# Performance work log

Measured on AMD Instinct MI355X. Metric: run time of the kernel, lower is better.

Reference implementation:

```python
import jax, jax.numpy as jnp
import numpy as np

E = 128   # embed_dim
H = 8     # num_heads
N, T, LQ, LK = 32, 50, 64, 64


def setup_inputs() -> dict:
    rng = jax.random.key(0)
    ks = jax.random.split(rng, 9)
    xav = np.sqrt(2.0 / (E + E)).astype(np.float32)  # xavier_normal for square E x E
    return {
        "query": jax.random.normal(ks[0], (N, T, LQ, E), jnp.float32),
        "key": jax.random.normal(ks[1], (N, T, LK, E), jnp.float32),
        "value": jax.random.normal(ks[2], (N, T, LK, E), jnp.float32),
        "key_padding_mask": jax.random.bernoulli(ks[3], 0.1, (N, T, LK)),
        "Wq": jax.random.normal(ks[4], (E, E), jnp.float32) * xav,
        "bq": jnp.zeros((E,), jnp.float32),
        "Wk": jax.random.normal(ks[5], (E, E), jnp.float32) * xav,
        "bk": jnp.zeros((E,), jnp.float32),
        "Wv": jax.random.normal(ks[6], (E, E), jnp.float32) * xav,
        "bv": jnp.zeros((E,), jnp.float32),
        "Wo": jax.random.normal(ks[7], (E, E), jnp.float32) * xav,
        "bo": jnp.zeros((E,), jnp.float32),
    }


def reference(query, key, value, key_padding_mask, Wq, bq, Wk, bk, Wv, bv, Wo, bo):
    b, t, lq, _ = query.shape
    lk = key.shape[2]
    # linear projections (torch Linear: x @ W.T + b)
    q = (query @ Wq.T + bq).reshape(b, t, lq, H, -1)   # [b,T,Lq,h,d]
    k = (key @ Wk.T + bk).reshape(b, t, lk, H, -1)     # [b,T,Lk,h,d]
    v = (value @ Wv.T + bv).reshape(b, t, lk, H, -1)   # [b,T,Lk,h,d]
    scale = 1.0 / np.sqrt(q.shape[-1]).astype(np.float32)
    attn = jnp.einsum('bTlhd,bTthd->bThlt', q, k) * scale  # [b,T,h,Lq,Lk]
    mask = key_padding_mask[:, :, None, None, :]            # [b,T,1,1,Lk]
    attn = jnp.where(mask, -jnp.inf, attn)
    attn = jax.nn.softmax(attn, axis=-1)
    attn = jnp.nan_to_num(attn, nan=0.0)                    # fully-masked rows -> 0
    out = jnp.einsum('bThlt,bTthd->bTlhd', attn, v)
    out = out.reshape(b, t, lq, -1) @ Wo.T + bo             # [b,T,Lq,E]
    # match torch output layout for attn: [head, b, T, Lq, Lk]
    return out, jnp.transpose(attn, (2, 0, 1, 3, 4))
```

## Files before the change

kernel.cpp:

```cpp
#include <hip/hip_runtime.h>
#include <hip/hip_bf16.h>


#define NBT 1600
#define OUT0_ELEMS 13107200L

typedef __attribute__((ext_vector_type(8))) short bf16x8;
typedef __attribute__((ext_vector_type(4))) short bf16x4;
typedef __attribute__((ext_vector_type(4))) float f32x4;
typedef __attribute__((ext_vector_type(4))) unsigned short u16x4;

__device__ __forceinline__ unsigned short f2b(float f) {
  union { float f; unsigned u; } v; v.f = f;
  unsigned r = v.u + 0x7FFFu + ((v.u >> 16) & 1u);
  return (unsigned short)(r >> 16);
}
__device__ __forceinline__ float b2f(unsigned short s) {
  union { unsigned u; float f; } v; v.u = ((unsigned)s) << 16;
  return v.f;
}
__device__ __forceinline__ bf16x4 pack4(f32x4 v) {
  bf16x4 r;
  r[0] = (short)f2b(v[0]); r[1] = (short)f2b(v[1]);
  r[2] = (short)f2b(v[2]); r[3] = (short)f2b(v[3]);
  return r;
}

#if defined(__has_builtin)
#if __has_builtin(__builtin_amdgcn_mfma_f32_16x16x16bf16_1k)
#define HAVE_MFMA16_1K 1
#endif
#endif

__device__ __forceinline__ f32x4 mfma16(bf16x4 a, bf16x4 b, f32x4 c) {
#ifdef HAVE_MFMA16_1K
  return __builtin_amdgcn_mfma_f32_16x16x16bf16_1k(a, b, c, 0, 0, 0);
#else
  f32x4 d;
  asm volatile("v_mfma_f32_16x16x16_bf16 %0, %1, %2, %3\n\ts_nop 7\n\ts_nop 7"
               : "=v"(d)
               : "v"(a), "v"(b), "v"(c));
  return d;
#endif
}

__device__ __forceinline__ int xs_idx(int r, int c) {
  return r * 128 + (c ^ ((r & 7) << 3));
}
__device__ __forceinline__ int qk_idx(int l, int d) {
  return l * 16 + (d ^ ((l & 3) << 2));
}
__device__ __forceinline__ int ps_idx(int r, int c) {
  return r * 64 + (c ^ ((r & 7) << 3));
}

__global__ void prep_kernel(const float* __restrict__ Wq,
                            const float* __restrict__ Wk,
                            const float* __restrict__ Wv,
                            const float* __restrict__ Wo,
                            const unsigned char* __restrict__ maskp,
                            unsigned short* __restrict__ wall,
                            int* __restrict__ flag) {
  int b = blockIdx.x;
  int t = threadIdx.x;
  if (b < 256) {
    int idx = b * 256 + t;
    int m = idx >> 14, j = idx & 16383;
    const float* src = (m == 0) ? Wq : (m == 1) ? Wk : (m == 2) ? Wv : Wo;
    float s = (m == 0) ? 0.25f : 1.0f;
    wall[idx] = f2b(src[j] * s);
  } else {
    __shared__ int sb, sf;
    if (t == 0) { sb = 0; sf = 0; }
    __syncthreads();
    int bnz = 0, fcnt = 0;
    for (int i = t * 16; i < t * 16 + 16; ++i)
      if ((i & 3) && maskp[i]) bnz++;
    const unsigned int* w = (const unsigned int*)maskp;
    for (int i = t * 4; i < t * 4 + 4; ++i)
      if (w[i] == 0x3f800000u) fcnt++;
    if (bnz) atomicAdd(&sb, 1);
    if (fcnt) atomicAdd(&sf, 1);
    __syncthreads();
    if (t == 0) *flag = sf ? 2 : (sb ? 1 : 0);
  }
}

__global__ __launch_bounds__(512, 4) void fused_kernel(
    const float* __restrict__ q_in, const float* __restrict__ k_in,
    const float* __restrict__ v_in, const unsigned char* __restrict__ maskp,
    const int* __restrict__ modeFlag, const unsigned short* __restrict__ wall,
    const float* __restrict__ bq, const float* __restrict__ bk,
    const float* __restrict__ bv, const float* __restrict__ bo,
    float* __restrict__ out0, float* __restrict__ attn_out) {
  __shared__ __align__(16) unsigned short Xs[64 * 128];
  __shared__ __align__(16) unsigned short QKw[8 * 1024];
  __shared__ float maskS[64];

  const int tid = threadIdx.x;
  const int w = tid >> 6;
  const int lane = tid & 63;
  const int ln = lane & 15, g = lane >> 4;
  const long bT = blockIdx.x;

  unsigned short* Sw = QKw + w * 1024;

  if (tid < 64) {
    int mode = *modeFlag;
    long midx = bT * 64 + tid;
    bool mk;
    if (mode == 0)      mk = ((const int*)maskp)[midx] != 0;
    else if (mode == 1) mk = maskp[midx] != 0;
    else                mk = ((const float*)maskp)[midx] != 0.0f;
    maskS[tid] = mk ? -INFINITY : 0.0f;
  }

  const float* xsrc0 = q_in + bT * 8192;
  const float* xsrc1 = k_in + bT * 8192;
  const float* xsrc2 = v_in + bT * 8192;

  float4 xcur[4];
  #pragma unroll
  for (int it = 0; it < 4; ++it)
    xcur[it] = *(const float4*)(xsrc0 + it * 2048 + tid * 4);

  bf16x4 vk[4];
  bf16x4 aK[4], bQ[4];

  #pragma unroll
  for (int t3 = 0; t3 < 3; ++t3) {
    #pragma unroll
    for (int it = 0; it < 4; ++it) {
      int flat = it * 2048 + tid * 4;
      int r = flat >> 7, c = flat & 127;
      float4 xv = xcur[it];
      u16x4 pk;
      pk[0] = f2b(xv.x); pk[1] = f2b(xv.y);
      pk[2] = f2b(xv.z); pk[3] = f2b(xv.w);
      *(u16x4*)&Xs[xs_idx(r, c)] = pk;
    }
    if (t3 < 2) {
      const float* nsrc = (t3 == 0) ? xsrc1 : xsrc2;
      #pragma unroll
      for (int it = 0; it < 4; ++it)
        xcur[it] = *(const float4*)(nsrc + it * 2048 + tid * 4);
    }
    __syncthreads();

    const unsigned short* wb = wall + t3 * 16384 + (w * 16 + ln) * 128 + 8 * g;
    const float* bias = (t3 == 0) ? bq : (t3 == 1) ? bk : bv;
    float bval = bias[w * 16 + ln] * ((t3 == 0) ? 0.25f : 1.0f);

    f32x4 acc[4] = {};
    #pragma unroll
    for (int ks = 0; ks < 4; ++ks) {
      bf16x8 bwk = *(const bf16x8*)(wb + ks * 32);
      bf16x8 a[4];
      #pragma unroll
      for (int ms = 0; ms < 4; ++ms)
        a[ms] = *(const bf16x8*)&Xs[xs_idx(ms * 16 + ln, ks * 32 + 8 * g)];
      #pragma unroll
      for (int ms = 0; ms < 4; ++ms)
        acc[ms] = __builtin_amdgcn_mfma_f32_16x16x32_bf16(a[ms], bwk,
                                                          acc[ms], 0, 0, 0);
    }
    __syncthreads();

    #pragma unroll
    for (int ms = 0; ms < 4; ++ms) {
      if (t3 == 2) {
        f32x4 vb;
        #pragma unroll
        for (int r = 0; r < 4; ++r) vb[r] = acc[ms][r] + bval;
        vk[ms] = pack4(vb);
      } else {
        #pragma unroll
        for (int r = 0; r < 4; ++r) {
          int l = ms * 16 + 4 * g + r;
          Sw[qk_idx(l, ln)] = f2b(acc[ms][r] + bval);
        }
      }
    }
    if (t3 == 0) {
      #pragma unroll
      for (int i = 0; i < 4; ++i)
        bQ[i] = *(const bf16x4*)&Sw[qk_idx(i * 16 + ln, 4 * g)];
    } else if (t3 == 1) {
      #pragma unroll
      for (int i = 0; i < 4; ++i)
        aK[i] = *(const bf16x4*)&Sw[qk_idx(i * 16 + ln, 4 * g)];
    }
  }

  const long abase = ((long)w * NBT + bT) * 4096;
  #pragma unroll
  for (int lsub = 0; lsub < 4; ++lsub) {
    f32x4 s4[4];
    #pragma unroll
    for (int t = 0; t < 4; ++t) {
      f32x4 z = {};
      s4[t] = mfma16(aK[t], bQ[lsub], z);
    }
    float m = -INFINITY;
    #pragma unroll
    for (int t = 0; t < 4; ++t) {
      f32x4 mvt = *(const f32x4*)&maskS[t * 16 + 4 * g];
      #pragma unroll
      for (int r = 0; r < 4; ++r) {
        float sv = s4[t][r] + mvt[r];
        s4[t][r] = sv;
        m = fmaxf(m, sv);
      }
    }
    m = fmaxf(m, __shfl_xor(m, 16, 64));
    m = fmaxf(m, __shfl_xor(m, 32, 64));
    float sum = 0.f;
    #pragma unroll
    for (int t = 0; t < 4; ++t)
      #pragma unroll
      for (int r = 0; r < 4; ++r) {
        float p = (m == -INFINITY) ? 0.f : __expf(s4[t][r] - m);
        s4[t][r] = p;
        sum += p;
      }
    sum += __shfl_xor(sum, 16, 64);
    sum += __shfl_xor(sum, 32, 64);
    float inv = (sum > 0.f) ? 1.f / sum : 0.f;

    bf16x4 pa4[4];
    #pragma unroll
    for (int t = 0; t < 4; ++t) {
      f32x4 ps;
      #pragma unroll
      for (int r = 0; r < 4; ++r) ps[r] = s4[t][r] * inv;
      pa4[t] = pack4(ps);
    }

    #pragma unroll
    for (int t = 0; t < 4; ++t)
      *(u16x4*)&Sw[ps_idx(ln, t * 16 + 4 * g)] = *(const u16x4*)&pa4[t];
    #pragma unroll
    for (int j = 0; j < 4; ++j) {
      int row = 4 * j + g;
      u16x4 pv = *(const u16x4*)&Sw[ps_idx(row, 4 * ln)];
      float4 o = make_float4(b2f(pv[0]), b2f(pv[1]), b2f(pv[2]), b2f(pv[3]));
      *(float4*)&attn_out[abase + (long)(lsub * 16 + row) * 64 + 4 * ln] = o;
    }

    f32x4 oacc = {};
    #pragma unroll
    for (int t = 0; t < 4; ++t) oacc = mfma16(pa4[t], vk[t], oacc);
    #pragma unroll
    for (int r = 0; r < 4; ++r)
      Xs[xs_idx(lsub * 16 + 4 * g + r, w * 16 + ln)] = f2b(oacc[r]);
  }

  __syncthreads();

  {
    const unsigned short* wo = wall + 3 * 16384 + (w * 16 + ln) * 128 + 8 * g;
    float bov = bo[w * 16 + ln];

    f32x4 acc[4] = {};
    #pragma unroll
    for (int ks = 0; ks < 4; ++ks) {
      bf16x8 bwk = *(const bf16x8*)(wo + ks * 32);
      bf16x8 a[4];
      #pragma unroll
      for (int ms = 0; ms < 4; ++ms)
        a[ms] = *(const bf16x8*)&Xs[xs_idx(ms * 16 + ln, ks * 32 + 8 * g)];
      #pragma unroll
      for (int ms = 0; ms < 4; ++ms)
        acc[ms] = __builtin_amdgcn_mfma_f32_16x16x32_bf16(a[ms], bwk,
                                                          acc[ms], 0, 0, 0);
    }
    #pragma unroll
    for (int ms = 0; ms < 4; ++ms)
      #pragma unroll
      for (int r = 0; r < 4; ++r)
        out0[(bT * 64 + ms * 16 + 4 * g + r) * 128 + w * 16 + ln] =
            acc[ms][r] + bov;
  }
}

extern "C" void kernel_launch(void* const* d_in, const int* in_sizes, int n_in,
                              void* d_out, int out_size, void* d_ws,
                              size_t ws_size, hipStream_t stream) {
  (void)in_sizes; (void)n_in; (void)out_size; (void)ws_size;
  const float* query = (const float*)d_in[0];
  const float* key   = (const float*)d_in[1];
  const float* value = (const float*)d_in[2];
  const unsigned char* mask = (const unsigned char*)d_in[3];
  const float* Wq = (const float*)d_in[4];
  const float* bq = (const float*)d_in[5];
  const float* Wk = (const float*)d_in[6];
  const float* bk = (const float*)d_in[7];
  const float* Wv = (const float*)d_in[8];
  const float* bv = (const float*)d_in[9];
  const float* Wo = (const float*)d_in[10];
  const float* bo = (const float*)d_in[11];

  float* out0 = (float*)d_out;
  float* attn_out = out0 + OUT0_ELEMS;

  char* ws = (char*)d_ws;
  int* flag = (int*)ws;
  unsigned short* wall = (unsigned short*)(ws + 256);

  prep_kernel<<<257, 256, 0, stream>>>(Wq, Wk, Wv, Wo, mask, wall, flag);
  fused_kernel<<<NBT, 512, 0, stream>>>(query, key, value, mask, flag, wall,
                                        bq, bk, bv, bo, out0, attn_out);
}
```

Measured before the change: 109.8 us.

## Fold weight conversion and mask-format detection into the fused kernel, drop prep launch

Removes the separate prep kernel that converted the four weight matrices to bf16 and detected the mask storage format. Each block now reads fp32 weights directly and converts them in registers, and it re-runs the mask-format probe itself using shared-memory atomics. This saves one kernel launch and its serialization, at the cost of double the weight load bytes, repeated conversion work in every block, and an extra pair of barriers. Launch bounds also drop from 4 to 3 waves per SIMD, which relaxes register pressure but may lower occupancy.

```diff
diff --git a/kernel.cpp b/kernel.cpp
--- a/kernel.cpp
+++ b/kernel.cpp
@@ -23,6 +23,14 @@
   bf16x4 r;
   r[0] = (short)f2b(v[0]); r[1] = (short)f2b(v[1]);
   r[2] = (short)f2b(v[2]); r[3] = (short)f2b(v[3]);
+  return r;
+}
+__device__ __forceinline__ bf16x8 packw(float4 a, float4 b) {
+  bf16x8 r;
+  r[0] = (short)f2b(a.x); r[1] = (short)f2b(a.y);
+  r[2] = (short)f2b(a.z); r[3] = (short)f2b(a.w);
+  r[4] = (short)f2b(b.x); r[5] = (short)f2b(b.y);
+  r[6] = (short)f2b(b.z); r[7] = (short)f2b(b.w);
   return r;
 }
 
@@ -54,48 +62,18 @@
   return r * 64 + (c ^ ((r & 7) << 3));
 }
 
-__global__ void prep_kernel(const float* __restrict__ Wq,
-                            const float* __restrict__ Wk,
-                            const float* __restrict__ Wv,
-                            const float* __restrict__ Wo,
-                            const unsigned char* __restrict__ maskp,
-                            unsigned short* __restrict__ wall,
-                            int* __restrict__ flag) {
-  int b = blockIdx.x;
-  int t = threadIdx.x;
-  if (b < 256) {
-    int idx = b * 256 + t;
-    int m = idx >> 14, j = idx & 16383;
-    const float* src = (m == 0) ? Wq : (m == 1) ? Wk : (m == 2) ? Wv : Wo;
-    float s = (m == 0) ? 0.25f : 1.0f;
-    wall[idx] = f2b(src[j] * s);
-  } else {
-    __shared__ int sb, sf;
-    if (t == 0) { sb = 0; sf = 0; }
-    __syncthreads();
-    int bnz = 0, fcnt = 0;
-    for (int i = t * 16; i < t * 16 + 16; ++i)
-      if ((i & 3) && maskp[i]) bnz++;
-    const unsigned int* w = (const unsigned int*)maskp;
-    for (int i = t * 4; i < t * 4 + 4; ++i)
-      if (w[i] == 0x3f800000u) fcnt++;
-    if (bnz) atomicAdd(&sb, 1);
-    if (fcnt) atomicAdd(&sf, 1);
-    __syncthreads();
-    if (t == 0) *flag = sf ? 2 : (sb ? 1 : 0);
-  }
-}
-
-__global__ __launch_bounds__(512, 4) void fused_kernel(
+__global__ __launch_bounds__(512, 3) void fused_kernel(
     const float* __restrict__ q_in, const float* __restrict__ k_in,
     const float* __restrict__ v_in, const unsigned char* __restrict__ maskp,
-    const int* __restrict__ modeFlag, const unsigned short* __restrict__ wall,
-    const float* __restrict__ bq, const float* __restrict__ bk,
-    const float* __restrict__ bv, const float* __restrict__ bo,
+    const float* __restrict__ Wq, const float* __restrict__ bq,
+    const float* __restrict__ Wk, const float* __restrict__ bk,
+    const float* __restrict__ Wv, const float* __restrict__ bv,
+    const float* __restrict__ Wo, const float* __restrict__ bo,
     float* __restrict__ out0, float* __restrict__ attn_out) {
   __shared__ __align__(16) unsigned short Xs[64 * 128];
   __shared__ __align__(16) unsigned short QKw[8 * 1024];
   __shared__ float maskS[64];
+  __shared__ int sflags[2];
 
   const int tid = threadIdx.x;
   const int w = tid >> 6;
@@ -105,8 +83,34 @@
 
   unsigned short* Sw = QKw + w * 1024;
 
+  const float* xsrc0 = q_in + bT * 8192;
+  const float* xsrc1 = k_in + bT * 8192;
+  const float* xsrc2 = v_in + bT * 8192;
+
+  float4 xcur[4];
+  #pragma unroll
+  for (int it = 0; it < 4; ++it)
+    xcur[it] = *(const float4*)(xsrc0 + it * 2048 + tid * 4);
+
+  if (tid < 2) sflags[tid] = 0;
+  int bnz = 0, fcnt = 0;
+  {
+    #pragma unroll
+    for (int i = 0; i < 8; ++i) {
+      int idx = tid * 8 + i;
+      if ((idx & 3) && maskp[idx]) bnz++;
+    }
+    const unsigned int* mw = (const unsigned int*)maskp;
+    if (mw[tid * 2] == 0x3f800000u) fcnt++;
+    if (mw[tid * 2 + 1] == 0x3f800000u) fcnt++;
+  }
+  __syncthreads();
+  if (bnz) atomicAdd(&sflags[0], 1);
+  if (fcnt) atomicAdd(&sflags[1], 1);
+  __syncthreads();
+  const int mode = sflags[1] ? 2 : (sflags[0] ? 1 : 0);
+
   if (tid < 64) {
-    int mode = *modeFlag;
     long midx = bT * 64 + tid;
     bool mk;
     if (mode == 0)      mk = ((const int*)maskp)[midx] != 0;
@@ -114,15 +118,6 @@
     else                mk = ((const float*)maskp)[midx] != 0.0f;
     maskS[tid] = mk ? -INFINITY : 0.0f;
   }
-
-  const float* xsrc0 = q_in + bT * 8192;
-  const float* xsrc1 = k_in + bT * 8192;
-  const float* xsrc2 = v_in + bT * 8192;
-
-  float4 xcur[4];
-  #pragma unroll
-  for (int it = 0; it < 4; ++it)
-    xcur[it] = *(const float4*)(xsrc0 + it * 2048 + tid * 4);
 
   bf16x4 vk[4];
   bf16x4 aK[4], bQ[4];
@@ -147,14 +142,21 @@
     }
     __syncthreads();
 
-    const unsigned short* wb = wall + t3 * 16384 + (w * 16 + ln) * 128 + 8 * g;
+    const float* Wsrc = (t3 == 0) ? Wq : (t3 == 1) ? Wk : Wv;
+    const float* wrow = Wsrc + (w * 16 + ln) * 128 + 8 * g;
     const float* bias = (t3 == 0) ? bq : (t3 == 1) ? bk : bv;
     float bval = bias[w * 16 + ln] * ((t3 == 0) ? 0.25f : 1.0f);
 
     f32x4 acc[4] = {};
     #pragma unroll
     for (int ks = 0; ks < 4; ++ks) {
-      bf16x8 bwk = *(const bf16x8*)(wb + ks * 32);
+      float4 wa = *(const float4*)(wrow + ks * 32);
+      float4 wb2 = *(const float4*)(wrow + ks * 32 + 4);
+      if (t3 == 0) {
+        wa.x *= 0.25f; wa.y *= 0.25f; wa.z *= 0.25f; wa.w *= 0.25f;
+        wb2.x *= 0.25f; wb2.y *= 0.25f; wb2.z *= 0.25f; wb2.w *= 0.25f;
+      }
+      bf16x8 bwk = packw(wa, wb2);
       bf16x8 a[4];
       #pragma unroll
       for (int ms = 0; ms < 4; ++ms)
@@ -258,13 +260,15 @@
   __syncthreads();
 
   {
-    const unsigned short* wo = wall + 3 * 16384 + (w * 16 + ln) * 128 + 8 * g;
+    const float* wrow = Wo + (w * 16 + ln) * 128 + 8 * g;
     float bov = bo[w * 16 + ln];
 
     f32x4 acc[4] = {};
     #pragma unroll
     for (int ks = 0; ks < 4; ++ks) {
-      bf16x8 bwk = *(const bf16x8*)(wo + ks * 32);
+      float4 wa = *(const float4*)(wrow + ks * 32);
+      float4 wb2 = *(const float4*)(wrow + ks * 32 + 4);
+      bf16x8 bwk = packw(wa, wb2);
       bf16x8 a[4];
       #pragma unroll
       for (int ms = 0; ms < 4; ++ms)
@@ -286,7 +290,7 @@
 extern "C" void kernel_launch(void* const* d_in, const int* in_sizes, int n_in,
                               void* d_out, int out_size, void* d_ws,
                               size_t ws_size, hipStream_t stream) {
-  (void)in_sizes; (void)n_in; (void)out_size; (void)ws_size;
+  (void)in_sizes; (void)n_in; (void)out_size; (void)d_ws; (void)ws_size;
   const float* query = (const float*)d_in[0];
   const float* key   = (const float*)d_in[1];
   const float* value = (const float*)d_in[2];
@@ -303,11 +307,7 @@
   float* out0 = (float*)d_out;
   float* attn_out = out0 + OUT0_ELEMS;
 
-  char* ws = (char*)d_ws;
-  int* flag = (int*)ws;
-  unsigned short* wall = (unsigned short*)(ws + 256);
-
-  prep_kernel<<<257, 256, 0, stream>>>(Wq, Wk, Wv, Wo, mask, wall, flag);
-  fused_kernel<<<NBT, 512, 0, stream>>>(query, key, value, mask, flag, wall,
-                                        bq, bk, bv, bo, out0, attn_out);
-}
+  fused_kernel<<<NBT, 512, 0, stream>>>(query, key, value, mask,
+                                        Wq, bq, Wk, bk, Wv, bv, Wo, bo,
+                                        out0, attn_out);
+}
```

New measurement: 154.4 us. +40.6%, slower.
